# Kernel optimization log

Measured on AMD Instinct MI355X. Metric: run time of the kernel, lower is better.

## Reference

```python
import jax, jax.numpy as jnp
import numpy as np

B, H, S, D = 1, 16, 4096, 64
TEMPERATURE = 8.0          # sqrt(d_k)
WINDOW_SIZE = 256
HALF_WINDOW = WINDOW_SIZE // 2
NEG_INF = -1000000000.0


def setup_inputs() -> dict:
    key = jax.random.key(0)
    kq, kk, kv = jax.random.split(key, 3)
    q = jax.random.normal(kq, (B, H, S, D), dtype=jnp.float32)
    k = jax.random.normal(kk, (B, H, S, D), dtype=jnp.float32)
    v = jax.random.normal(kv, (B, H, S, D), dtype=jnp.float32)
    return {"q": q, "k": k, "v": v}


def reference(q, k, v):
    # q,k,v: [B,H,S,D]
    seq = q.shape[2]
    attn = jnp.einsum('bhqd,bhkd->bhqk', q, k) / TEMPERATURE  # [B,H,S,S]
    if seq > WINDOW_SIZE:
        idx = jnp.arange(seq)
        # torch loop: row i allows columns [i-half, i+half] inclusive
        win = jnp.abs(idx[:, None] - idx[None, :]) <= HALF_WINDOW  # [S,S]
        attn = jnp.where(win[None, None, :, :], attn, NEG_INF)
    attn = jax.nn.softmax(attn, axis=-1)  # dropout p=0 -> identity
    out = jnp.einsum('bhqk,bhkd->bhqd', attn, v)
    return (out, attn)
```

## Files before the change

kernel.cpp:

```cpp
#include <hip/hip_runtime.h>
#include <hip/hip_bf16.h>


typedef short bf16x8 __attribute__((ext_vector_type(8)));
typedef float f32x4  __attribute__((ext_vector_type(4)));
typedef unsigned int u32;
typedef unsigned short u16;

namespace {
constexpr int S = 4096, H = 16, Dh = 64, TR = 16, HW = 128, NCH = 5;
constexpr int UW  = NCH * 64;
constexpr int KP  = 72;
constexpr int PBW = UW + 8;
constexpr int NTILE = H * (S / TR);
constexpr int KBUF = 2 * 64 * KP;
}

__device__ __forceinline__ u16 f2bf(float x) {
    u32 u = __float_as_uint(x);
    return (u16)((u + 0x7fffu + ((u >> 16) & 1u)) >> 16);
}
__device__ __forceinline__ float bf2f(u16 h) {
    return __uint_as_float(((u32)h) << 16);
}

__device__ __forceinline__ void bar_lds() {
    asm volatile("s_waitcnt lgkmcnt(0)" ::: "memory");
    __builtin_amdgcn_s_barrier();
    asm volatile("" ::: "memory");
}

__global__ __launch_bounds__(256, 3)
void wattn(const float* __restrict__ q, const float* __restrict__ k,
           const float* __restrict__ v, float* __restrict__ out,
           float* __restrict__ attn)
{
    __shared__ __align__(16) u16 hbuf[2 * KBUF + TR * PBW];
    __shared__ float red[TR * 4];
    __shared__ float inv_row[TR];
    u16* pb_ = hbuf + 2 * KBUF;

    const int tid  = threadIdx.x;
    const int wave = tid >> 6, lane = tid & 63;
    const int g = lane >> 4, m = lane & 15;

    int bx = blockIdx.x;
    bx = (bx & 7) * (NTILE / 8) + (bx >> 3);
    const int h  = bx >> 8;
    const int r0 = (bx & 255) * TR;
    const int c0 = max(0, r0 - HW);
    const int c1 = min(S - 1, r0 + TR - 1 + HW);
    const int c0q = c0 >> 2;

    const float* qp = q + ((size_t)h * S + r0) * Dh;
    const float* kp = k + (size_t)h * S * Dh;
    const float* vp = v + (size_t)h * S * Dh;
    float* arow = attn + ((size_t)h * S + r0) * S;

    bf16x8 aqh[2], aql[2];
    #pragma unroll
    for (int ks = 0; ks < 2; ++ks) {
        const float* qsrc = qp + m * Dh + ks * 32 + g * 8;
        float4 t0 = *(const float4*)(qsrc);
        float4 t1 = *(const float4*)(qsrc + 4);
        float xs[8] = {t0.x, t0.y, t0.z, t0.w, t1.x, t1.y, t1.z, t1.w};
        #pragma unroll
        for (int i = 0; i < 8; ++i) {
            u16 hi = f2bf(xs[i]);
            aqh[ks][i] = (short)hi;
            aql[ks][i] = (short)f2bf(xs[i] - bf2f(hi));
        }
    }

    const int col = tid >> 2, d16 = (tid & 3) * 16;
    float4 rk[4];
    {
        const float* src = kp + (size_t)min(c0 + col, S - 1) * Dh + d16;
        #pragma unroll
        for (int i4 = 0; i4 < 4; ++i4) rk[i4] = *(const float4*)(src + i4 * 4);
    }
    f32x4 sc[NCH];
    #pragma unroll
    for (int cc = 0; cc < NCH; ++cc) {
        u16* kh = hbuf + (cc & 1) * KBUF;
        u16* kl = kh + 64 * KP;
        {
            u16* dh = kh + col * KP + d16;
            u16* dl = kl + col * KP + d16;
            #pragma unroll
            for (int i4 = 0; i4 < 4; ++i4) {
                float xs[4] = {rk[i4].x, rk[i4].y, rk[i4].z, rk[i4].w};
                #pragma unroll
                for (int i = 0; i < 4; ++i) {
                    u16 hi = f2bf(xs[i]);
                    dh[i4 * 4 + i] = hi;
                    dl[i4 * 4 + i] = f2bf(xs[i] - bf2f(hi));
                }
            }
        }
        if (cc + 1 < NCH) {
            const float* src =
                kp + (size_t)min(c0 + (cc + 1) * 64 + col, S - 1) * Dh + d16;
            #pragma unroll
            for (int i4 = 0; i4 < 4; ++i4) rk[i4] = *(const float4*)(src + i4 * 4);
        }
        bar_lds();
        f32x4 acc = {0.f, 0.f, 0.f, 0.f};
        #pragma unroll
        for (int ks = 0; ks < 2; ++ks) {
            bf16x8 bh = *(const bf16x8*)(kh + (wave * 16 + m) * KP + ks * 32 + g * 8);
            bf16x8 bl = *(const bf16x8*)(kl + (wave * 16 + m) * KP + ks * 32 + g * 8);
            acc = __builtin_amdgcn_mfma_f32_16x16x32_bf16(aqh[ks], bh, acc, 0, 0, 0);
            acc = __builtin_amdgcn_mfma_f32_16x16x32_bf16(aql[ks], bh, acc, 0, 0, 0);
            acc = __builtin_amdgcn_mfma_f32_16x16x32_bf16(aqh[ks], bl, acc, 0, 0, 0);
        }
        sc[cc] = acc;
    }

    const int j = tid & 63, dbase = (tid >> 6) * 16;
    float4 rv[4];
    {
        const float* src = vp + (size_t)min(c0 + j, S - 1) * Dh + dbase;
        #pragma unroll
        for (int i4 = 0; i4 < 4; ++i4) rv[i4] = *(const float4*)(src + i4 * 4);
    }

    float rs[4] = {0.f, 0.f, 0.f, 0.f};
    #pragma unroll
    for (int cc = 0; cc < NCH; ++cc) {
        const int colg = c0 + cc * 64 + wave * 16 + m;
        #pragma unroll
        for (int w = 0; w < 4; ++w) {
            const int row = r0 + g * 4 + w;
            const float l = sc[cc][w] * 0.125f;
            const bool ok = (colg >= row - HW) && (colg <= row + HW) && (colg <= c1);
            const float ev = ok ? __expf(l) : 0.f;
            rs[w] += ev;
            pb_[(g * 4 + w) * PBW + cc * 64 + wave * 16 + m] = f2bf(ev);
        }
    }
    #pragma unroll
    for (int off = 1; off < 16; off <<= 1) {
        #pragma unroll
        for (int w = 0; w < 4; ++w) rs[w] += __shfl_xor(rs[w], off, 64);
    }
    if (m == 0) {
        #pragma unroll
        for (int w = 0; w < 4; ++w) red[(g * 4 + w) * 4 + wave] = rs[w];
    }
    bar_lds();
    if (tid < TR) {
        float4 p4 = *(const float4*)(red + tid * 4);
        inv_row[tid] = 1.0f / (p4.x + p4.y + p4.z + p4.w);
    }
    bar_lds();

    f32x4 oacc = {0.f, 0.f, 0.f, 0.f};
    #pragma unroll
    for (int cc = 0; cc < NCH; ++cc) {
        u16* vt = hbuf + (cc & 1) * KBUF;
        #pragma unroll
        for (int i4 = 0; i4 < 4; ++i4) {
            float xs[4] = {rv[i4].x, rv[i4].y, rv[i4].z, rv[i4].w};
            #pragma unroll
            for (int i = 0; i < 4; ++i)
                vt[(dbase + i4 * 4 + i) * KP + j] = f2bf(xs[i]);
        }
        if (cc + 1 < NCH) {
            const float* src = vp + (size_t)min(c0 + (cc + 1) * 64 + j, S - 1) * Dh + dbase;
            #pragma unroll
            for (int i4 = 0; i4 < 4; ++i4) rv[i4] = *(const float4*)(src + i4 * 4);
        }
        bar_lds();
        #pragma unroll
        for (int ks = 0; ks < 2; ++ks) {
            bf16x8 ap = *(const bf16x8*)(pb_ + m * PBW + cc * 64 + ks * 32 + g * 8);
            bf16x8 bv = *(const bf16x8*)(vt + (wave * 16 + m) * KP + ks * 32 + g * 8);
            oacc = __builtin_amdgcn_mfma_f32_16x16x32_bf16(ap, bv, oacc, 0, 0, 0);
        }
    }

    {
        float4 inv4 = *(const float4*)(inv_row + g * 4);
        float* op = out + (((size_t)h * S + r0 + g * 4) * Dh) + wave * 16 + m;
        #pragma unroll
        for (int w = 0; w < 4; ++w) {
            const float iw = (w == 0) ? inv4.x : (w == 1) ? inv4.y : (w == 2) ? inv4.z : inv4.w;
            op[(size_t)w * Dh] = oacc[w] * iw;
        }
    }

    {
        for (int r = 0; r < TR; ++r) {
            const float inv = inv_row[r];
            float4* dst = (float4*)(arow + (size_t)r * S);
            #pragma unroll
            for (int kk4 = 0; kk4 < 4; ++kk4) {
                const int c4 = tid + 256 * kk4;
                const int o4 = c4 - c0q;
                float4 val = {0.f, 0.f, 0.f, 0.f};
                if ((unsigned)o4 < (unsigned)(UW / 4)) {
                    ushort4 hh = *(const ushort4*)(pb_ + r * PBW + o4 * 4);
                    val.x = bf2f(hh.x) * inv; val.y = bf2f(hh.y) * inv;
                    val.z = bf2f(hh.z) * inv; val.w = bf2f(hh.w) * inv;
                }
                dst[c4] = val;
            }
        }
    }
}

extern "C" void kernel_launch(void* const* d_in, const int* in_sizes, int n_in,
                              void* d_out, int out_size, void* d_ws, size_t ws_size,
                              hipStream_t stream) {
    const float* q = (const float*)d_in[0];
    const float* k = (const float*)d_in[1];
    const float* v = (const float*)d_in[2];
    float* out  = (float*)d_out;
    float* attn = out + (size_t)H * S * Dh;
    wattn<<<dim3(NTILE), dim3(256), 0, stream>>>(q, k, v, out, attn);
}
```

Baseline: 1.093 ms.

## Fuse QK and PV into one chunk loop over 64-row tiles with streaming zero stores

```diff
diff --git a/kernel.cpp b/kernel.cpp
--- a/kernel.cpp
+++ b/kernel.cpp
@@ -8,12 +8,9 @@
 typedef unsigned short u16;
 
 namespace {
-constexpr int S = 4096, H = 16, Dh = 64, TR = 16, HW = 128, NCH = 5;
-constexpr int UW  = NCH * 64;
+constexpr int S = 4096, H = 16, Dh = 64, TRB = 64, HW = 128, NCH = 5;
 constexpr int KP  = 72;
-constexpr int PBW = UW + 8;
-constexpr int NTILE = H * (S / TR);
-constexpr int KBUF = 2 * 64 * KP;
+constexpr int NTILE = H * (S / TRB);
 }
 
 __device__ __forceinline__ u16 f2bf(float x) {
@@ -30,15 +27,17 @@
     asm volatile("" ::: "memory");
 }
 
-__global__ __launch_bounds__(256, 3)
+__global__ __launch_bounds__(256, 4)
 void wattn(const float* __restrict__ q, const float* __restrict__ k,
            const float* __restrict__ v, float* __restrict__ out,
            float* __restrict__ attn)
 {
-    __shared__ __align__(16) u16 hbuf[2 * KBUF + TR * PBW];
-    __shared__ float red[TR * 4];
-    __shared__ float inv_row[TR];
-    u16* pb_ = hbuf + 2 * KBUF;
+    __shared__ __align__(16) u16 hbuf[4 * 64 * KP];
+    __shared__ float inv_row[TRB];
+    u16* kh_ = hbuf;
+    u16* kl_ = hbuf + 64 * KP;
+    u16* vt_ = hbuf + 2 * 64 * KP;
+    u16* pc_ = hbuf + 3 * 64 * KP;
 
     const int tid  = threadIdx.x;
     const int wave = tid >> 6, lane = tid & 63;
@@ -46,10 +45,10 @@
 
     int bx = blockIdx.x;
     bx = (bx & 7) * (NTILE / 8) + (bx >> 3);
-    const int h  = bx >> 8;
-    const int r0 = (bx & 255) * TR;
+    const int h  = bx >> 6;
+    const int r0 = (bx & 63) * TRB;
     const int c0 = max(0, r0 - HW);
-    const int c1 = min(S - 1, r0 + TR - 1 + HW);
+    const int c1 = min(S - 1, r0 + TRB - 1 + HW);
     const int c0q = c0 >> 2;
 
     const float* qp = q + ((size_t)h * S + r0) * Dh;
@@ -60,7 +59,7 @@
     bf16x8 aqh[2], aql[2];
     #pragma unroll
     for (int ks = 0; ks < 2; ++ks) {
-        const float* qsrc = qp + m * Dh + ks * 32 + g * 8;
+        const float* qsrc = qp + (wave * 16 + m) * Dh + ks * 32 + g * 8;
         float4 t0 = *(const float4*)(qsrc);
         float4 t1 = *(const float4*)(qsrc + 4);
         float xs[8] = {t0.x, t0.y, t0.z, t0.w, t1.x, t1.y, t1.z, t1.w};
@@ -72,21 +71,30 @@
         }
     }
 
-    const int col = tid >> 2, d16 = (tid & 3) * 16;
-    float4 rk[4];
+    const int kcol = tid >> 2, kd = (tid & 3) * 16;
+    const int vj = tid & 63, vd = (tid >> 6) * 16;
+
+    float4 rk[4], rv[4];
     {
-        const float* src = kp + (size_t)min(c0 + col, S - 1) * Dh + d16;
+        const float* src = kp + (size_t)min(c0 + kcol, S - 1) * Dh + kd;
         #pragma unroll
         for (int i4 = 0; i4 < 4; ++i4) rk[i4] = *(const float4*)(src + i4 * 4);
     }
-    f32x4 sc[NCH];
-    #pragma unroll
+    {
+        const float* src = vp + (size_t)min(c0 + vj, S - 1) * Dh + vd;
+        #pragma unroll
+        for (int i4 = 0; i4 < 4; ++i4) rv[i4] = *(const float4*)(src + i4 * 4);
+    }
+
+    float rs[4] = {0.f, 0.f, 0.f, 0.f};
+    f32x4 oacc[4] = {{0.f,0.f,0.f,0.f},{0.f,0.f,0.f,0.f},
+                     {0.f,0.f,0.f,0.f},{0.f,0.f,0.f,0.f}};
+
     for (int cc = 0; cc < NCH; ++cc) {
-        u16* kh = hbuf + (cc & 1) * KBUF;
-        u16* kl = kh + 64 * KP;
+        if (cc) bar_lds();
         {
-            u16* dh = kh + col * KP + d16;
-            u16* dl = kl + col * KP + d16;
+            u16* dh = kh_ + kcol * KP + kd;
+            u16* dl = kl_ + kcol * KP + kd;
             #pragma unroll
             for (int i4 = 0; i4 < 4; ++i4) {
                 float xs[4] = {rk[i4].x, rk[i4].y, rk[i4].z, rk[i4].w};
@@ -98,114 +106,126 @@
                 }
             }
         }
+        #pragma unroll
+        for (int i4 = 0; i4 < 4; ++i4) {
+            float xs[4] = {rv[i4].x, rv[i4].y, rv[i4].z, rv[i4].w};
+            #pragma unroll
+            for (int i = 0; i < 4; ++i)
+                vt_[(vd + i4 * 4 + i) * KP + vj] = f2bf(xs[i]);
+        }
+        {
+            const f32x4 z4 = {0.f, 0.f, 0.f, 0.f};
+            const int rbeg = cc * 13;
+            const int rend = (cc == NCH - 1) ? TRB : rbeg + 13;
+            for (int r = rbeg; r < rend; ++r) {
+                f32x4* dst = (f32x4*)(arow + (size_t)r * S);
+                #pragma unroll
+                for (int kk4 = 0; kk4 < 4; ++kk4) {
+                    const int c4 = tid + 256 * kk4;
+                    if ((unsigned)(c4 - c0q) >= (unsigned)(TRB + 2 * HW) / 4)
+                        __builtin_nontemporal_store(z4, dst + c4);
+                }
+            }
+        }
         if (cc + 1 < NCH) {
-            const float* src =
-                kp + (size_t)min(c0 + (cc + 1) * 64 + col, S - 1) * Dh + d16;
-            #pragma unroll
-            for (int i4 = 0; i4 < 4; ++i4) rk[i4] = *(const float4*)(src + i4 * 4);
+            const float* srck = kp + (size_t)min(c0 + (cc + 1) * 64 + kcol, S - 1) * Dh + kd;
+            const float* srcv = vp + (size_t)min(c0 + (cc + 1) * 64 + vj,   S - 1) * Dh + vd;
+            #pragma unroll
+            for (int i4 = 0; i4 < 4; ++i4) {
+                rk[i4] = *(const float4*)(srck + i4 * 4);
+                rv[i4] = *(const float4*)(srcv + i4 * 4);
+            }
         }
         bar_lds();
-        f32x4 acc = {0.f, 0.f, 0.f, 0.f};
-        #pragma unroll
-        for (int ks = 0; ks < 2; ++ks) {
-            bf16x8 bh = *(const bf16x8*)(kh + (wave * 16 + m) * KP + ks * 32 + g * 8);
-            bf16x8 bl = *(const bf16x8*)(kl + (wave * 16 + m) * KP + ks * 32 + g * 8);
-            acc = __builtin_amdgcn_mfma_f32_16x16x32_bf16(aqh[ks], bh, acc, 0, 0, 0);
-            acc = __builtin_amdgcn_mfma_f32_16x16x32_bf16(aql[ks], bh, acc, 0, 0, 0);
-            acc = __builtin_amdgcn_mfma_f32_16x16x32_bf16(aqh[ks], bl, acc, 0, 0, 0);
-        }
-        sc[cc] = acc;
-    }
-
-    const int j = tid & 63, dbase = (tid >> 6) * 16;
-    float4 rv[4];
-    {
-        const float* src = vp + (size_t)min(c0 + j, S - 1) * Dh + dbase;
-        #pragma unroll
-        for (int i4 = 0; i4 < 4; ++i4) rv[i4] = *(const float4*)(src + i4 * 4);
-    }
-
-    float rs[4] = {0.f, 0.f, 0.f, 0.f};
-    #pragma unroll
-    for (int cc = 0; cc < NCH; ++cc) {
-        const int colg = c0 + cc * 64 + wave * 16 + m;
-        #pragma unroll
-        for (int w = 0; w < 4; ++w) {
-            const int row = r0 + g * 4 + w;
-            const float l = sc[cc][w] * 0.125f;
-            const bool ok = (colg >= row - HW) && (colg <= row + HW) && (colg <= c1);
-            const float ev = ok ? __expf(l) : 0.f;
-            rs[w] += ev;
-            pb_[(g * 4 + w) * PBW + cc * 64 + wave * 16 + m] = f2bf(ev);
-        }
-    }
+        f32x4 acc[4] = {{0.f,0.f,0.f,0.f},{0.f,0.f,0.f,0.f},
+                        {0.f,0.f,0.f,0.f},{0.f,0.f,0.f,0.f}};
+        #pragma unroll
+        for (int ci = 0; ci < 4; ++ci) {
+            #pragma unroll
+            for (int ks = 0; ks < 2; ++ks) {
+                bf16x8 bh = *(const bf16x8*)(kh_ + (ci * 16 + m) * KP + ks * 32 + g * 8);
+                bf16x8 bl = *(const bf16x8*)(kl_ + (ci * 16 + m) * KP + ks * 32 + g * 8);
+                acc[ci] = __builtin_amdgcn_mfma_f32_16x16x32_bf16(aqh[ks], bh, acc[ci], 0, 0, 0);
+                acc[ci] = __builtin_amdgcn_mfma_f32_16x16x32_bf16(aql[ks], bh, acc[ci], 0, 0, 0);
+                acc[ci] = __builtin_amdgcn_mfma_f32_16x16x32_bf16(aqh[ks], bl, acc[ci], 0, 0, 0);
+            }
+        }
+        #pragma unroll
+        for (int ci = 0; ci < 4; ++ci) {
+            const int colg = c0 + cc * 64 + ci * 16 + m;
+            #pragma unroll
+            for (int w = 0; w < 4; ++w) {
+                const int row = r0 + wave * 16 + g * 4 + w;
+                const float l = acc[ci][w] * 0.125f;
+                const bool ok = (colg >= row - HW) && (colg <= row + HW) && (colg <= c1);
+                const float ev = ok ? __expf(l) : 0.f;
+                rs[w] += ev;
+                pc_[(wave * 16 + g * 4 + w) * KP + ci * 16 + m] = f2bf(ev);
+            }
+        }
+        bar_lds();
+        {
+            const int br = tid >> 2, bc = tid & 3;
+            #pragma unroll
+            for (int it = 0; it < 4; ++it) {
+                const int c = bc + 4 * it;
+                const int col4 = c0q + cc * 16 + c;
+                if (col4 < S / 4) {
+                    ushort4 hh = *(const ushort4*)(pc_ + br * KP + c * 4);
+                    float4 val;
+                    val.x = bf2f(hh.x); val.y = bf2f(hh.y);
+                    val.z = bf2f(hh.z); val.w = bf2f(hh.w);
+                    ((float4*)(arow + (size_t)br * S))[col4] = val;
+                }
+            }
+        }
+        #pragma unroll
+        for (int di = 0; di < 4; ++di) {
+            #pragma unroll
+            for (int ks = 0; ks < 2; ++ks) {
+                bf16x8 ap = *(const bf16x8*)(pc_ + (wave * 16 + m) * KP + ks * 32 + g * 8);
+                bf16x8 bv = *(const bf16x8*)(vt_ + (di * 16 + m) * KP + ks * 32 + g * 8);
+                oacc[di] = __builtin_amdgcn_mfma_f32_16x16x32_bf16(ap, bv, oacc[di], 0, 0, 0);
+            }
+        }
+    }
+
     #pragma unroll
     for (int off = 1; off < 16; off <<= 1) {
         #pragma unroll
         for (int w = 0; w < 4; ++w) rs[w] += __shfl_xor(rs[w], off, 64);
     }
+    float invw[4];
+    #pragma unroll
+    for (int w = 0; w < 4; ++w) invw[w] = 1.0f / rs[w];
     if (m == 0) {
         #pragma unroll
-        for (int w = 0; w < 4; ++w) red[(g * 4 + w) * 4 + wave] = rs[w];
-    }
+        for (int w = 0; w < 4; ++w) inv_row[wave * 16 + g * 4 + w] = invw[w];
+    }
+
+    {
+        float* ob = out + ((size_t)h * S + r0 + wave * 16) * Dh;
+        #pragma unroll
+        for (int di = 0; di < 4; ++di)
+            #pragma unroll
+            for (int w = 0; w < 4; ++w)
+                ob[(g * 4 + w) * Dh + di * 16 + m] = oacc[di][w] * invw[w];
+    }
+
+    asm volatile("s_waitcnt vmcnt(0)" ::: "memory");
     bar_lds();
-    if (tid < TR) {
-        float4 p4 = *(const float4*)(red + tid * 4);
-        inv_row[tid] = 1.0f / (p4.x + p4.y + p4.z + p4.w);
-    }
-    bar_lds();
-
-    f32x4 oacc = {0.f, 0.f, 0.f, 0.f};
-    #pragma unroll
-    for (int cc = 0; cc < NCH; ++cc) {
-        u16* vt = hbuf + (cc & 1) * KBUF;
-        #pragma unroll
-        for (int i4 = 0; i4 < 4; ++i4) {
-            float xs[4] = {rv[i4].x, rv[i4].y, rv[i4].z, rv[i4].w};
-            #pragma unroll
-            for (int i = 0; i < 4; ++i)
-                vt[(dbase + i4 * 4 + i) * KP + j] = f2bf(xs[i]);
-        }
-        if (cc + 1 < NCH) {
-            const float* src = vp + (size_t)min(c0 + (cc + 1) * 64 + j, S - 1) * Dh + dbase;
-            #pragma unroll
-            for (int i4 = 0; i4 < 4; ++i4) rv[i4] = *(const float4*)(src + i4 * 4);
-        }
-        bar_lds();
-        #pragma unroll
-        for (int ks = 0; ks < 2; ++ks) {
-            bf16x8 ap = *(const bf16x8*)(pb_ + m * PBW + cc * 64 + ks * 32 + g * 8);
-            bf16x8 bv = *(const bf16x8*)(vt + (wave * 16 + m) * KP + ks * 32 + g * 8);
-            oacc = __builtin_amdgcn_mfma_f32_16x16x32_bf16(ap, bv, oacc, 0, 0, 0);
-        }
-    }
-
-    {
-        float4 inv4 = *(const float4*)(inv_row + g * 4);
-        float* op = out + (((size_t)h * S + r0 + g * 4) * Dh) + wave * 16 + m;
-        #pragma unroll
-        for (int w = 0; w < 4; ++w) {
-            const float iw = (w == 0) ? inv4.x : (w == 1) ? inv4.y : (w == 2) ? inv4.z : inv4.w;
-            op[(size_t)w * Dh] = oacc[w] * iw;
-        }
-    }
-
-    {
-        for (int r = 0; r < TR; ++r) {
-            const float inv = inv_row[r];
-            float4* dst = (float4*)(arow + (size_t)r * S);
-            #pragma unroll
-            for (int kk4 = 0; kk4 < 4; ++kk4) {
-                const int c4 = tid + 256 * kk4;
-                const int o4 = c4 - c0q;
-                float4 val = {0.f, 0.f, 0.f, 0.f};
-                if ((unsigned)o4 < (unsigned)(UW / 4)) {
-                    ushort4 hh = *(const ushort4*)(pb_ + r * PBW + o4 * 4);
-                    val.x = bf2f(hh.x) * inv; val.y = bf2f(hh.y) * inv;
-                    val.z = bf2f(hh.z) * inv; val.w = bf2f(hh.w) * inv;
-                }
-                dst[c4] = val;
-            }
+    #pragma unroll 4
+    for (int it = 0; it < 20; ++it) {
+        const int idx = tid + 256 * it;
+        const int r = idx / 80;
+        const int c = idx - r * 80;
+        const int col4 = c0q + c;
+        if (col4 < S / 4) {
+            float4* p = (float4*)(arow + (size_t)r * S) + col4;
+            float4 t = *p;
+            const float iv = inv_row[r];
+            t.x *= iv; t.y *= iv; t.z *= iv; t.w *= iv;
+            *p = t;
         }
     }
 }
```

Result: slower. 1.122 ms (+2.6%).
